# Kernel tuning notes

Hardware: AMD Instinct MI355X
Metric: run time of the kernel (lower is better)

Reference implementation:

```python
import jax, jax.numpy as jnp
import numpy as np

E = 1024  # embedding == hidden size
L = 2     # layer_num
S = 128   # sentence_length == seq_len
B = 64
LABEL = 5


def setup_inputs() -> dict:
    key = jax.random.key(0)
    ks = jax.random.split(key, 20)
    sc = 1.0 / np.sqrt(2 * E)
    def lin(k, i, o):
        kw, kb = jax.random.split(k)
        return (jax.random.uniform(kw, (i, o), jnp.float32, -sc, sc),
                jax.random.uniform(kb, (o,), jnp.float32, -sc, sc))
    # per-direction stacked gate weights [L, 2E, E]
    def gates(k):
        kk = jax.random.split(k, 3 * L)
        Ws, bs = [], []
        for g in range(3):
            W = jnp.stack([lin(kk[g * L + l], 2 * E, E)[0] for l in range(L)])
            b = jnp.stack([lin(jax.random.fold_in(kk[g * L + l], 7), 2 * E, E)[1] for l in range(L)])
            Ws.append(W); bs.append(b)
        return Ws, bs
    (fW, fb) = gates(ks[0])
    (bW, bb) = gates(ks[1])
    word_W, word_b = lin(ks[2], 2 * E, 1)
    pw = 1.0 / np.sqrt(S)
    pred_W = jax.random.uniform(ks[3], (S, LABEL), jnp.float32, -pw, pw)
    pred_b = jax.random.uniform(ks[4], (LABEL,), jnp.float32, -pw, pw)
    return {
        "inputs": jax.random.normal(ks[5], (B, S, E), jnp.float32),
        "cell_states": jnp.zeros((B, E), jnp.float32),
        "hidden_states": jnp.zeros((B, E), jnp.float32),
        "back_states": jnp.zeros((B, E), jnp.float32),
        "back_hidden": jnp.zeros((B, E), jnp.float32),
        "fWf": fW[0], "fbf": fb[0], "fWi": fW[1], "fbi": fb[1], "fWc": fW[2], "fbc": fb[2],
        "bWf": bW[0], "bbf": bb[0], "bWi": bW[1], "bbi": bb[1], "bWc": bW[2], "bbc": bb[2],
        "word_W": word_W, "word_b": word_b, "pred_W": pred_W, "pred_b": pred_b,
    }


def _run_dir(x_seq, h0, c0, Wf, bf, Wi, bi, Wc, bc):
    # x_seq: [S,B,E]; h0,c0: [B,E] broadcast to all layers
    hc0 = (jnp.broadcast_to(h0, (L,) + h0.shape), jnp.broadcast_to(c0, (L,) + c0.shape))
    def step(carry, x_t):
        h, c = carry
        inp = x_t
        hs, cs = [], []
        for l in range(L):
            z = jnp.concatenate([h[l], inp], axis=-1)       # [B,2E]
            f = jax.nn.sigmoid(z @ Wf[l] + bf[l])
            i = jax.nn.sigmoid(z @ Wi[l] + bi[l])
            g = jnp.tanh(z @ Wc[l] + bc[l])
            c_new = c[l] * f + i * g
            h_new = jnp.tanh(c_new) * f                     # note: forget gate reused as output gate (as in source)
            hs.append(h_new); cs.append(c_new); inp = h_new
        return (jnp.stack(hs), jnp.stack(cs)), inp
    _, out = jax.lax.scan(step, hc0, x_seq)
    return out  # [S,B,E]


def reference(inputs, cell_states, hidden_states, back_states, back_hidden,
              fWf, fbf, fWi, fbi, fWc, fbc,
              bWf, bbf, bWi, bbi, bWc, bbc,
              word_W, word_b, pred_W, pred_b):
    x = jnp.transpose(inputs, (1, 0, 2))                     # [S,B,E]
    fwd = _run_dir(x, hidden_states, cell_states, fWf, fbf, fWi, fbi, fWc, fbc)
    bwd = _run_dir(x[::-1], hidden_states, cell_states, bWf, bbf, bWi, bbi, bWc, bbc)[::-1]
    out = jnp.concatenate([fwd, bwd], axis=-1)               # [S,B,2E]
    out = jnp.transpose(out, (1, 0, 2))                      # [B,S,2E]
    w = (out @ word_W + word_b).reshape(out.shape[0], -1)    # [B,S]
    return w @ pred_W + pred_b                               # [B,LABEL]
```

## Files before the change

kernel.cpp:

```cpp
#include <hip/hip_runtime.h>
#include <cstddef>
#include <cstdint>

typedef _Float16 half8 __attribute__((ext_vector_type(8)));
typedef float f32x4 __attribute__((ext_vector_type(4)));

#define S_LEN 128
#define B_SZ  64
#define E_SZ  1024
#define NLBL  5
#define NPHASE 129

#define WOFF_WREC  0ull
#define WOFF_WINP  25165824ull
#define WOFF_X16   50331648ull
#define M0_H0    67108864ull
#define M0_H1    100925440ull
#define M0_WPART 134742016ull
#define M0_W     138936320ull
#define M0_FLAGS 138969088ull
#define NEED0    139001856ull
#define M1_H0    67108864ull
#define M1_H1    67633152ull
#define M1_WPART 68157440ull
#define M1_W     72351744ull
#define M1_FLAGS 72384512ull
#define NEED1    72417280ull

struct PP {
  const float* x;
  const float* W[2][3];
  const float* bias[2][3];
  const float* wordW;
  const float* cs0;
  _Float16* wrec;
  _Float16* winp;
  _Float16* x16;
  _Float16* h0;
  _Float16* h1;
  float* w;
  float* wpart;
  int* flags;
};

__device__ __forceinline__ uint32_t pack2f16(float a, float b) {
  return (uint32_t)__builtin_bit_cast(unsigned short, (_Float16)a) |
         ((uint32_t)__builtin_bit_cast(unsigned short, (_Float16)b) << 16);
}

#define MFMA16(A, B, C) __builtin_amdgcn_mfma_f32_16x16x32_f16(A, B, C, 0, 0, 0)

#define S_ISSUE_A4C(Q, P0, P1, P2, P3)                                     \
  asm volatile("global_load_dwordx4 %0, %4, off sc0 sc1\n\t"               \
               "global_load_dwordx4 %1, %5, off sc0 sc1\n\t"               \
               "global_load_dwordx4 %2, %6, off sc0 sc1\n\t"               \
               "global_load_dwordx4 %3, %7, off sc0 sc1"                   \
               : "=&v"((Q)[0]), "=&v"((Q)[1]), "=&v"((Q)[2]), "=&v"((Q)[3]) \
               : "v"(P0), "v"(P1), "v"(P2), "v"(P3))

#define S_ISSUE_A4P(Q, P0, P1, P2, P3)                                     \
  asm volatile("global_load_dwordx4 %0, %4, off\n\t"                       \
               "global_load_dwordx4 %1, %5, off\n\t"                       \
               "global_load_dwordx4 %2, %6, off\n\t"                       \
               "global_load_dwordx4 %3, %7, off"                           \
               : "=&v"((Q)[0]), "=&v"((Q)[1]), "=&v"((Q)[2]), "=&v"((Q)[3]) \
               : "v"(P0), "v"(P1), "v"(P2), "v"(P3))

#define S_WAITV(N)                                                         \
  asm volatile("s_waitcnt vmcnt(" #N ")" ::: "memory");                    \
  __builtin_amdgcn_sched_barrier(0)

__device__ __forceinline__ void comp_rec2s(const uint4* q, int kcA,
                                           const _Float16* wlds, int l64,
                                           f32x4 acc[3][2]) {
  #pragma unroll
  for (int s = 0; s < 2; ++s) {
    const int kc = kcA + s;
    const half8 a0 = __builtin_bit_cast(half8, q[s * 2 + 0]);
    const half8 a1 = __builtin_bit_cast(half8, q[s * 2 + 1]);
    #pragma unroll
    for (int g = 0; g < 3; ++g) {
      const half8 bf = *(const half8*)(wlds + ((size_t)(g * 32 + kc) * 64 + l64) * 8);
      acc[g][0] = MFMA16(a0, bf, acc[g][0]);
      acc[g][1] = MFMA16(a1, bf, acc[g][1]);
    }
  }
}

__device__ __forceinline__ void comp_inp2(const uint4* aq, const uint4* wq,
                                          f32x4 acc[3][2]) {
  #pragma unroll
  for (int s = 0; s < 2; ++s) {
    const half8 a0 = __builtin_bit_cast(half8, aq[s * 2 + 0]);
    const half8 a1 = __builtin_bit_cast(half8, aq[s * 2 + 1]);
    #pragma unroll
    for (int g = 0; g < 3; ++g) {
      const half8 bf = __builtin_bit_cast(half8, wq[s * 3 + g]);
      acc[g][0] = MFMA16(a0, bf, acc[g][0]);
      acc[g][1] = MFMA16(a1, bf, acc[g][1]);
    }
  }
}

__global__ __launch_bounds__(256)
void conv_w_kernel(PP p) {
  const int blk = blockIdx.x;
  const int part = blk & 1;
  const int j16 = (blk >> 1) & 63;
  const int rest = blk >> 7;
  const int g = rest % 3;
  const int dl = rest / 3;
  const int l = dl & 1, d = dl >> 1;
  const int tid = threadIdx.x;
  const int l2 = tid & 63, kc0 = tid >> 6;
  const float* W = p.W[d][g] + (size_t)l * 2048 * 1024 + (size_t)(part ? 1024 : 0) * 1024;
  _Float16* out = (part ? p.winp : p.wrec) + (size_t)(dl * 64 + j16) * 49152 + (size_t)g * 16384;
  const int j = j16 * 16 + (l2 & 15);
  const int kbase = (l2 >> 4) * 8;
  #pragma unroll
  for (int ki = 0; ki < 8; ++ki) {
    const int kc = kc0 * 8 + ki;
    const int k0 = kc * 32 + kbase;
    half8 h;
    #pragma unroll
    for (int e2 = 0; e2 < 8; ++e2) h[e2] = (_Float16)W[(size_t)(k0 + e2) * 1024 + j];
    *(half8*)(out + ((size_t)kc * 64 + l2) * 8) = h;
  }
}

__global__ __launch_bounds__(256)
void conv_x_kernel(const float* x, _Float16* x16) {
  const size_t i8 = ((size_t)blockIdx.x * 256 + threadIdx.x) * 8;
  float4 a = *(const float4*)(x + i8);
  float4 b = *(const float4*)(x + i8 + 4);
  half8 h;
  h[0] = (_Float16)a.x; h[1] = (_Float16)a.y; h[2] = (_Float16)a.z; h[3] = (_Float16)a.w;
  h[4] = (_Float16)b.x; h[5] = (_Float16)b.y; h[6] = (_Float16)b.z; h[7] = (_Float16)b.w;
  *(half8*)(x16 + i8) = h;
}

template<int MODE>
__global__ __launch_bounds__(256)
void init2_kernel(PP p, const float* hs) {
  const size_t HU = (MODE == 0) ? 65536 : 131072;
  const size_t i = (size_t)blockIdx.x * 256 + threadIdx.x;
  if (i < 2 * HU) {
    const size_t ai = (i < HU) ? i : i - HU;
    _Float16* dst = (i < HU) ? p.h0 : p.h1;
    const size_t grp = ai >> 15;
    const size_t be = ai & 32767;
    const size_t b = be >> 9, ec = be & 511;
    const uint32_t v = pack2f16(hs[b * 1024 + ec * 2], hs[b * 1024 + ec * 2 + 1]);
    const size_t u32off = (MODE == 0) ? (grp * 129 * 32768 + be) : (grp * 32768 + be);
    ((uint32_t*)dst)[u32off] = v;
  } else if (i < 2 * HU + 8192) {
    p.flags[i - 2 * HU] = 0;
  }
}

template<int MODE>
__global__ __launch_bounds__(512, 2)
void lstm_persist(PP p) {
  extern __shared__ char smem[];
  _Float16* wlds = (_Float16*)smem;
  float* pre  = (float*)(smem + 98304);
  float* wred = (float*)(smem + 150528);

  const int tid = threadIdx.x;
  const int l64 = tid & 63, lr = l64 & 15, lg = l64 >> 4;
  const int wv = tid >> 6, kq = wv & 3, mg = wv >> 2;
  const int blk = blockIdx.x;
  const int j16 = blk & 63, l = (blk >> 6) & 1, d = blk >> 7;
  const int idx = blk & 127;
  const int j0 = j16 * 16;

  if (tid == 0)
    (void)__hip_atomic_load(p.flags, __ATOMIC_ACQUIRE, __HIP_MEMORY_SCOPE_AGENT);
  __syncthreads();

  const size_t tileoff = (size_t)((d * 2 + l) * 64 + j16) * 49152;
  {
    const float4* src = (const float4*)(p.wrec + tileoff);
    float4* dst = (float4*)wlds;
    #pragma unroll
    for (int i = 0; i < 12; ++i) dst[tid + i * 512] = src[tid + i * 512];
  }
  const _Float16* wtile = p.winp + tileoff;
  _Float16* hrec_arr = l ? p.h1 : p.h0;

  uint4 wreg[24];
  #pragma unroll
  for (int i = 0; i < 24; ++i) {
    const int kcl = i / 3, g = i % 3;
    const int kc = kq * 8 + kcl;
    wreg[i] = *(const uint4*)(wtile + ((size_t)(g * 32 + kc) * 64 + l64) * 8);
  }

  const int pr = tid >> 3;
  const int pj = (tid & 7) * 2;
  const int pjg = j0 + pj;
  const float bsf0 = p.bias[d][0][l * E_SZ + pjg], bsf1 = p.bias[d][0][l * E_SZ + pjg + 1];
  const float bsi0 = p.bias[d][1][l * E_SZ + pjg], bsi1 = p.bias[d][1][l * E_SZ + pjg + 1];
  const float bsc0 = p.bias[d][2][l * E_SZ + pjg], bsc1 = p.bias[d][2][l * E_SZ + pjg + 1];
  const float ww0 = p.wordW[d * E_SZ + pjg], ww1 = p.wordW[d * E_SZ + pjg + 1];
  float creg0 = p.cs0[(size_t)pr * E_SZ + pjg];
  float creg1 = p.cs0[(size_t)pr * E_SZ + pjg + 1];
  __syncthreads();

  auto hoff = [&](int dd, int s) -> size_t {
    return (MODE == 0) ? ((size_t)dd * 129 + s) * 65536 : ((size_t)(dd * 2 + s)) * 65536;
  };

  for (int ph = 0; ph < NPHASE; ++ph) {
    const int t = l ? (ph - 1) : ph;
    if ((unsigned)t < (unsigned)S_LEN) {
      const int par = t & 1, prev = par ^ 1;
      const int td = d ? (S_LEN - 1 - t) : t;
      const int rs    = (MODE == 0) ? t : prev;
      const int wslot = (MODE == 0) ? (t + 1) : par;
      const int islot = (MODE == 0) ? (t + 1) : par;

      const _Float16* hAf = hrec_arr + hoff(d, rs);
      const _Float16* r0 = hAf + (size_t)(mg * 32 + lr) * 1024;
      const _Float16* r1 = hAf + (size_t)(mg * 32 + 16 + lr) * 1024;
      const _Float16* a0base;
      const _Float16* a1base;
      if (l == 0) {
        a0base = p.x16 + ((size_t)(mg * 32 + lr) * S_LEN + td) * 1024;
        a1base = p.x16 + ((size_t)(mg * 32 + 16 + lr) * S_LEN + td) * 1024;
      } else {
        const _Float16* hf = p.h0 + hoff(d, islot);
        a0base = hf + (size_t)(mg * 32 + lr) * 1024;
        a1base = hf + (size_t)(mg * 32 + 16 + lr) * 1024;
      }

      const f32x4 zero = {0.f, 0.f, 0.f, 0.f};
      f32x4 acc[3][2];
      #pragma unroll
      for (int g = 0; g < 3; ++g) { acc[g][0] = zero; acc[g][1] = zero; }

      auto issue_rec = [&](int c, uint4* Q) {
        const int kk = (kq * 8 + c * 2) * 32 + lg * 8;
        if (MODE == 0) {
          S_ISSUE_A4P(Q, r0 + kk, r1 + kk, r0 + kk + 32, r1 + kk + 32);
        } else {
          S_ISSUE_A4C(Q, r0 + kk, r1 + kk, r0 + kk + 32, r1 + kk + 32);
        }
      };
      auto issue_a = [&](int c, uint4* Q) {
        const int kk = (kq * 8 + c * 2) * 32 + lg * 8;
        if (MODE == 0 || l == 0) {
          S_ISSUE_A4P(Q, a0base + kk, a1base + kk, a0base + kk + 32, a1base + kk + 32);
        } else {
          S_ISSUE_A4C(Q, a0base + kk, a1base + kk, a0base + kk + 32, a1base + kk + 32);
        }
      };

      uint4 b0[4], b1[4], b2[4];
      issue_rec(0, b0); issue_rec(1, b1); issue_rec(2, b2);
      S_WAITV(8); comp_rec2s(b0, kq * 8 + 0, wlds, l64, acc); issue_rec(3, b0);
      S_WAITV(8); comp_rec2s(b1, kq * 8 + 2, wlds, l64, acc); issue_a(0, b1);
      S_WAITV(8); comp_rec2s(b2, kq * 8 + 4, wlds, l64, acc); issue_a(1, b2);
      S_WAITV(8); comp_rec2s(b0, kq * 8 + 6, wlds, l64, acc); issue_a(2, b0);
      S_WAITV(8); comp_inp2(b1, &wreg[0],  acc); issue_a(3, b1);
      S_WAITV(8); comp_inp2(b2, &wreg[6],  acc);
      S_WAITV(4); comp_inp2(b0, &wreg[12], acc);
      S_WAITV(0); comp_inp2(b1, &wreg[18], acc);

      #pragma unroll
      for (int g = 0; g < 3; ++g)
        #pragma unroll
        for (int mt = 0; mt < 2; ++mt)
          #pragma unroll
          for (int pp = 0; pp < 4; ++pp)
            pre[(((kq * 3 + g) * 64) + (mg * 2 + mt) * 16 + lg * 4 + pp) * 17 + lr] =
                acc[g][mt][pp];
      __syncthreads();

      float fp0 = bsf0, fp1 = bsf1, ip0 = bsi0, ip1 = bsi1, cp0 = bsc0, cp1 = bsc1;
      #pragma unroll
      for (int k = 0; k < 4; ++k) {
        fp0 += pre[((k * 3 + 0) * 64 + pr) * 17 + pj];
        fp1 += pre[((k * 3 + 0) * 64 + pr) * 17 + pj + 1];
        ip0 += pre[((k * 3 + 1) * 64 + pr) * 17 + pj];
        ip1 += pre[((k * 3 + 1) * 64 + pr) * 17 + pj + 1];
        cp0 += pre[((k * 3 + 2) * 64 + pr) * 17 + pj];
        cp1 += pre[((k * 3 + 2) * 64 + pr) * 17 + pj + 1];
      }
      const float fg0 = 1.f / (1.f + expf(-fp0)), fg1 = 1.f / (1.f + expf(-fp1));
      const float ig0 = 1.f / (1.f + expf(-ip0)), ig1 = 1.f / (1.f + expf(-ip1));
      const float gg0 = tanhf(cp0), gg1 = tanhf(cp1);
      creg0 = creg0 * fg0 + ig0 * gg0;
      creg1 = creg1 * fg1 + ig1 * gg1;
      const float h0v = tanhf(creg0) * fg0;
      const float h1v = tanhf(creg1) * fg1;

      uint32_t* hdst = (uint32_t*)(hrec_arr + hoff(d, wslot) + (size_t)pr * 1024 + pjg);
      const uint32_t pk = pack2f16(h0v, h1v);
      asm volatile("global_store_dword %0, %1, off sc0 sc1" ::"v"(hdst), "v"(pk) : "memory");
      if (l) {
        wred[pr * 16 + pj] = h0v * ww0;
        wred[pr * 16 + pj + 1] = h1v * ww1;
        __syncthreads();
        if (tid < 64) {
          float s = 0.f;
          #pragma unroll
          for (int q = 0; q < 16; ++q) s += wred[tid * 16 + q];
          p.wpart[((size_t)(d * 64 + j16) * S_LEN + td) * 64 + tid] = s;
        }
      }
    }

    __syncthreads();
    if (tid == 0) {
      __hip_atomic_store(p.flags + (size_t)(d * 128 + idx) * 32, ph + 1,
                         __ATOMIC_RELAXED, __HIP_MEMORY_SCOPE_AGENT);
      asm volatile("s_waitcnt vmcnt(0)" ::: "memory");
    }
    if (tid < 128) {
      const int* fl = p.flags + (size_t)(d * 128 + tid) * 32;
      int f, it = 0;
      do {
        f = __hip_atomic_load(fl, __ATOMIC_RELAXED, __HIP_MEMORY_SCOPE_AGENT);
        if (f >= ph + 1) break;
        __builtin_amdgcn_s_sleep(1);
      } while (++it < (1 << 22));
    }
    __syncthreads();
  }
}

__global__ __launch_bounds__(64)
void reduce_w_kernel(const float* wpart, const float* wordb, float* w) {
  const int t = blockIdx.x, b = threadIdx.x;
  float s = wordb[0];
  #pragma unroll 8
  for (int q = 0; q < 128; ++q)
    s += wpart[((size_t)q * S_LEN + t) * 64 + b];
  w[b * S_LEN + t] = s;
}

__global__ __launch_bounds__(320)
void final_kernel(const float* w, const float* predW, const float* predb, float* out) {
  const int tid = threadIdx.x;
  if (tid >= B_SZ * NLBL) return;
  const int b = tid / NLBL, lab = tid % NLBL;
  float s = predb[lab];
  #pragma unroll 8
  for (int t = 0; t < S_LEN; ++t) s += w[b * S_LEN + t] * predW[t * NLBL + lab];
  out[tid] = s;
}

extern "C" void kernel_launch(void* const* d_in, const int* in_sizes, int n_in,
                              void* d_out, int out_size, void* d_ws, size_t ws_size,
                              hipStream_t stream) {
  char* ws = (char*)d_ws;
  const bool hist = (ws_size >= NEED0);

  PP p;
  p.x = (const float*)d_in[0];
  p.W[0][0] = (const float*)d_in[5];  p.bias[0][0] = (const float*)d_in[6];
  p.W[0][1] = (const float*)d_in[7];  p.bias[0][1] = (const float*)d_in[8];
  p.W[0][2] = (const float*)d_in[9];  p.bias[0][2] = (const float*)d_in[10];
  p.W[1][0] = (const float*)d_in[11]; p.bias[1][0] = (const float*)d_in[12];
  p.W[1][1] = (const float*)d_in[13]; p.bias[1][1] = (const float*)d_in[14];
  p.W[1][2] = (const float*)d_in[15]; p.bias[1][2] = (const float*)d_in[16];
  p.wordW = (const float*)d_in[17];
  p.cs0   = (const float*)d_in[1];
  p.wrec  = (_Float16*)(ws + WOFF_WREC);
  p.winp  = (_Float16*)(ws + WOFF_WINP);
  p.x16   = (_Float16*)(ws + WOFF_X16);
  if (hist) {
    p.h0    = (_Float16*)(ws + M0_H0);
    p.h1    = (_Float16*)(ws + M0_H1);
    p.wpart = (float*)(ws + M0_WPART);
    p.w     = (float*)(ws + M0_W);
    p.flags = (int*)(ws + M0_FLAGS);
  } else {
    p.h0    = (_Float16*)(ws + M1_H0);
    p.h1    = (_Float16*)(ws + M1_H1);
    p.wpart = (float*)(ws + M1_WPART);
    p.w     = (float*)(ws + M1_W);
    p.flags = (int*)(ws + M1_FLAGS);
  }

  hipFuncSetAttribute(reinterpret_cast<const void*>(&lstm_persist<0>),
                      hipFuncAttributeMaxDynamicSharedMemorySize, 155648);
  hipFuncSetAttribute(reinterpret_cast<const void*>(&lstm_persist<1>),
                      hipFuncAttributeMaxDynamicSharedMemorySize, 155648);

  conv_w_kernel<<<1536, 256, 0, stream>>>(p);
  conv_x_kernel<<<4096, 256, 0, stream>>>(p.x, p.x16);
  if (hist) {
    init2_kernel<0><<<544, 256, 0, stream>>>(p, (const float*)d_in[2]);
    lstm_persist<0><<<256, 512, 155648, stream>>>(p);
  } else {
    init2_kernel<1><<<1056, 256, 0, stream>>>(p, (const float*)d_in[2]);
    lstm_persist<1><<<256, 512, 155648, stream>>>(p);
  }
  reduce_w_kernel<<<128, 64, 0, stream>>>(p.wpart, (const float*)d_in[18], p.w);
  final_kernel<<<1, 320, 0, stream>>>(p.w, (const float*)d_in[19],
                                      (const float*)d_in[20], (float*)d_out);
}
```

Measured before the change: 1.360 ms.

## Prefetch next-step x before barrier, publish flags early, narrow waits, fast activations

Layer-0 blocks now prefetch half of the next timestep's input x before the inter-block spin wait. The first two input-projection MFMA chunks then run from registers while the recurrent loads are still in flight. The flag store now happens right after the gate math, before the word-projection partial reduction, and layer-0 blocks in MODE 0 wait only on the 64 layer-0 flags. Sigmoid and tanh use __expf-based approximations. Together these aim to shorten the serialized per-step critical path of the persistent recurrent kernel, at some cost in activation accuracy and register pressure.

```diff
diff --git a/kernel.cpp b/kernel.cpp
--- a/kernel.cpp
+++ b/kernel.cpp
@@ -46,6 +46,13 @@
 __device__ __forceinline__ uint32_t pack2f16(float a, float b) {
   return (uint32_t)__builtin_bit_cast(unsigned short, (_Float16)a) |
          ((uint32_t)__builtin_bit_cast(unsigned short, (_Float16)b) << 16);
+}
+
+__device__ __forceinline__ float fast_sigmoid(float x) {
+  return 1.f / (1.f + __expf(-x));
+}
+__device__ __forceinline__ float fast_tanh(float x) {
+  return 1.f - 2.f / (__expf(2.f * x) + 1.f);
 }
 
 #define MFMA16(A, B, C) __builtin_amdgcn_mfma_f32_16x16x32_f16(A, B, C, 0, 0, 0)
@@ -211,9 +218,24 @@
     return (MODE == 0) ? ((size_t)dd * 129 + s) * 65536 : ((size_t)(dd * 2 + s)) * 65536;
   };
 
+  const _Float16* xr0 = p.x16 + (size_t)(mg * 32 + lr) * S_LEN * 1024;
+  const _Float16* xr1 = p.x16 + (size_t)(mg * 32 + 16 + lr) * S_LEN * 1024;
+
+  uint4 xq0[4], xq1[4];
+  if (l == 0) {
+    const int tdn = d ? (S_LEN - 1) : 0;
+    const _Float16* a0 = xr0 + (size_t)tdn * 1024;
+    const _Float16* a1 = xr1 + (size_t)tdn * 1024;
+    const int kk0 = (kq * 8 + 0) * 32 + lg * 8;
+    const int kk1 = (kq * 8 + 2) * 32 + lg * 8;
+    S_ISSUE_A4P(xq0, a0 + kk0, a1 + kk0, a0 + kk0 + 32, a1 + kk0 + 32);
+    S_ISSUE_A4P(xq1, a0 + kk1, a1 + kk1, a0 + kk1 + 32, a1 + kk1 + 32);
+  }
+
   for (int ph = 0; ph < NPHASE; ++ph) {
     const int t = l ? (ph - 1) : ph;
-    if ((unsigned)t < (unsigned)S_LEN) {
+    const bool active = (unsigned)t < (unsigned)S_LEN;
+    if (active) {
       const int par = t & 1, prev = par ^ 1;
       const int td = d ? (S_LEN - 1 - t) : t;
       const int rs    = (MODE == 0) ? t : prev;
@@ -223,16 +245,6 @@
       const _Float16* hAf = hrec_arr + hoff(d, rs);
       const _Float16* r0 = hAf + (size_t)(mg * 32 + lr) * 1024;
       const _Float16* r1 = hAf + (size_t)(mg * 32 + 16 + lr) * 1024;
-      const _Float16* a0base;
-      const _Float16* a1base;
-      if (l == 0) {
-        a0base = p.x16 + ((size_t)(mg * 32 + lr) * S_LEN + td) * 1024;
-        a1base = p.x16 + ((size_t)(mg * 32 + 16 + lr) * S_LEN + td) * 1024;
-      } else {
-        const _Float16* hf = p.h0 + hoff(d, islot);
-        a0base = hf + (size_t)(mg * 32 + lr) * 1024;
-        a1base = hf + (size_t)(mg * 32 + 16 + lr) * 1024;
-      }
 
       const f32x4 zero = {0.f, 0.f, 0.f, 0.f};
       f32x4 acc[3][2];
@@ -247,25 +259,46 @@
           S_ISSUE_A4C(Q, r0 + kk, r1 + kk, r0 + kk + 32, r1 + kk + 32);
         }
       };
-      auto issue_a = [&](int c, uint4* Q) {
-        const int kk = (kq * 8 + c * 2) * 32 + lg * 8;
-        if (MODE == 0 || l == 0) {
+
+      uint4 b0[4], b1[4], b2[4];
+      if (l == 0) {
+        const _Float16* a0base = xr0 + (size_t)td * 1024;
+        const _Float16* a1base = xr1 + (size_t)td * 1024;
+        auto issue_x = [&](int c, uint4* Q) {
+          const int kk = (kq * 8 + c * 2) * 32 + lg * 8;
           S_ISSUE_A4P(Q, a0base + kk, a1base + kk, a0base + kk + 32, a1base + kk + 32);
-        } else {
-          S_ISSUE_A4C(Q, a0base + kk, a1base + kk, a0base + kk + 32, a1base + kk + 32);
-        }
-      };
-
-      uint4 b0[4], b1[4], b2[4];
-      issue_rec(0, b0); issue_rec(1, b1); issue_rec(2, b2);
-      S_WAITV(8); comp_rec2s(b0, kq * 8 + 0, wlds, l64, acc); issue_rec(3, b0);
-      S_WAITV(8); comp_rec2s(b1, kq * 8 + 2, wlds, l64, acc); issue_a(0, b1);
-      S_WAITV(8); comp_rec2s(b2, kq * 8 + 4, wlds, l64, acc); issue_a(1, b2);
-      S_WAITV(8); comp_rec2s(b0, kq * 8 + 6, wlds, l64, acc); issue_a(2, b0);
-      S_WAITV(8); comp_inp2(b1, &wreg[0],  acc); issue_a(3, b1);
-      S_WAITV(8); comp_inp2(b2, &wreg[6],  acc);
-      S_WAITV(4); comp_inp2(b0, &wreg[12], acc);
-      S_WAITV(0); comp_inp2(b1, &wreg[18], acc);
+        };
+        issue_rec(0, b0); issue_rec(1, b1); issue_rec(2, b2);
+        comp_inp2(xq0, &wreg[0], acc);
+        comp_inp2(xq1, &wreg[6], acc);
+        S_WAITV(8);  comp_rec2s(b0, kq * 8 + 0, wlds, l64, acc); issue_rec(3, b0);
+        S_WAITV(8);  comp_rec2s(b1, kq * 8 + 2, wlds, l64, acc); issue_x(2, b1);
+        S_WAITV(8);  comp_rec2s(b2, kq * 8 + 4, wlds, l64, acc); issue_x(3, b2);
+        S_WAITV(8);  comp_rec2s(b0, kq * 8 + 6, wlds, l64, acc);
+        S_WAITV(4);  comp_inp2(b1, &wreg[12], acc);
+        S_WAITV(0);  comp_inp2(b2, &wreg[18], acc);
+      } else {
+        const _Float16* hf = p.h0 + hoff(d, islot);
+        const _Float16* a0base = hf + (size_t)(mg * 32 + lr) * 1024;
+        const _Float16* a1base = hf + (size_t)(mg * 32 + 16 + lr) * 1024;
+        auto issue_a = [&](int c, uint4* Q) {
+          const int kk = (kq * 8 + c * 2) * 32 + lg * 8;
+          if (MODE == 0) {
+            S_ISSUE_A4P(Q, a0base + kk, a1base + kk, a0base + kk + 32, a1base + kk + 32);
+          } else {
+            S_ISSUE_A4C(Q, a0base + kk, a1base + kk, a0base + kk + 32, a1base + kk + 32);
+          }
+        };
+        issue_rec(0, b0); issue_rec(1, b1); issue_rec(2, b2);
+        S_WAITV(8); comp_rec2s(b0, kq * 8 + 0, wlds, l64, acc); issue_rec(3, b0);
+        S_WAITV(8); comp_rec2s(b1, kq * 8 + 2, wlds, l64, acc); issue_a(0, b1);
+        S_WAITV(8); comp_rec2s(b2, kq * 8 + 4, wlds, l64, acc); issue_a(1, b2);
+        S_WAITV(8); comp_rec2s(b0, kq * 8 + 6, wlds, l64, acc); issue_a(2, b0);
+        S_WAITV(8); comp_inp2(b1, &wreg[0],  acc); issue_a(3, b1);
+        S_WAITV(8); comp_inp2(b2, &wreg[6],  acc);
+        S_WAITV(4); comp_inp2(b0, &wreg[12], acc);
+        S_WAITV(0); comp_inp2(b1, &wreg[18], acc);
+      }
 
       #pragma unroll
       for (int g = 0; g < 3; ++g)
@@ -287,13 +320,13 @@
         cp0 += pre[((k * 3 + 2) * 64 + pr) * 17 + pj];
         cp1 += pre[((k * 3 + 2) * 64 + pr) * 17 + pj + 1];
       }
-      const float fg0 = 1.f / (1.f + expf(-fp0)), fg1 = 1.f / (1.f + expf(-fp1));
-      const float ig0 = 1.f / (1.f + expf(-ip0)), ig1 = 1.f / (1.f + expf(-ip1));
-      const float gg0 = tanhf(cp0), gg1 = tanhf(cp1);
+      const float fg0 = fast_sigmoid(fp0), fg1 = fast_sigmoid(fp1);
+      const float ig0 = fast_sigmoid(ip0), ig1 = fast_sigmoid(ip1);
+      const float gg0 = fast_tanh(cp0), gg1 = fast_tanh(cp1);
       creg0 = creg0 * fg0 + ig0 * gg0;
       creg1 = creg1 * fg1 + ig1 * gg1;
-      const float h0v = tanhf(creg0) * fg0;
-      const float h1v = tanhf(creg1) * fg1;
+      const float h0v = fast_tanh(creg0) * fg0;
+      const float h1v = fast_tanh(creg1) * fg1;
 
       uint32_t* hdst = (uint32_t*)(hrec_arr + hoff(d, wslot) + (size_t)pr * 1024 + pjg);
       const uint32_t pk = pack2f16(h0v, h1v);
@@ -301,30 +334,51 @@
       if (l) {
         wred[pr * 16 + pj] = h0v * ww0;
         wred[pr * 16 + pj + 1] = h1v * ww1;
-        __syncthreads();
-        if (tid < 64) {
-          float s = 0.f;
-          #pragma unroll
-          for (int q = 0; q < 16; ++q) s += wred[tid * 16 + q];
-          p.wpart[((size_t)(d * 64 + j16) * S_LEN + td) * 64 + tid] = s;
-        }
+      }
+      __syncthreads();
+      if (tid == 0) {
+        __hip_atomic_store(p.flags + (size_t)(d * 128 + idx) * 32, ph + 1,
+                           __ATOMIC_RELAXED, __HIP_MEMORY_SCOPE_AGENT);
+        asm volatile("s_waitcnt vmcnt(0)" ::: "memory");
+      }
+      if (l && tid < 64) {
+        const int tdw = d ? (S_LEN - 1 - t) : t;
+        float s = 0.f;
+        #pragma unroll
+        for (int q = 0; q < 16; ++q) s += wred[tid * 16 + q];
+        p.wpart[((size_t)(d * 64 + j16) * S_LEN + tdw) * 64 + tid] = s;
+      }
+    } else {
+      __syncthreads();
+      if (tid == 0) {
+        __hip_atomic_store(p.flags + (size_t)(d * 128 + idx) * 32, ph + 1,
+                           __ATOMIC_RELAXED, __HIP_MEMORY_SCOPE_AGENT);
+        asm volatile("s_waitcnt vmcnt(0)" ::: "memory");
       }
     }
 
-    __syncthreads();
-    if (tid == 0) {
-      __hip_atomic_store(p.flags + (size_t)(d * 128 + idx) * 32, ph + 1,
-                         __ATOMIC_RELAXED, __HIP_MEMORY_SCOPE_AGENT);
-      asm volatile("s_waitcnt vmcnt(0)" ::: "memory");
+    if (l == 0 && ph + 1 < S_LEN) {
+      const int tn = ph + 1;
+      const int tdn = d ? (S_LEN - 1 - tn) : tn;
+      const _Float16* a0 = xr0 + (size_t)tdn * 1024;
+      const _Float16* a1 = xr1 + (size_t)tdn * 1024;
+      const int kk0 = (kq * 8 + 0) * 32 + lg * 8;
+      const int kk1 = (kq * 8 + 2) * 32 + lg * 8;
+      S_ISSUE_A4P(xq0, a0 + kk0, a1 + kk0, a0 + kk0 + 32, a1 + kk0 + 32);
+      S_ISSUE_A4P(xq1, a0 + kk1, a1 + kk1, a0 + kk1 + 32, a1 + kk1 + 32);
     }
-    if (tid < 128) {
-      const int* fl = p.flags + (size_t)(d * 128 + tid) * 32;
-      int f, it = 0;
-      do {
-        f = __hip_atomic_load(fl, __ATOMIC_RELAXED, __HIP_MEMORY_SCOPE_AGENT);
-        if (f >= ph + 1) break;
-        __builtin_amdgcn_s_sleep(1);
-      } while (++it < (1 << 22));
+
+    {
+      const int nflags = (MODE == 0 && l == 0) ? 64 : 128;
+      if (tid < nflags) {
+        const int* fl = p.flags + (size_t)(d * 128 + tid) * 32;
+        int f, it = 0;
+        do {
+          f = __hip_atomic_load(fl, __ATOMIC_RELAXED, __HIP_MEMORY_SCOPE_AGENT);
+          if (f >= ph + 1) break;
+          __builtin_amdgcn_s_sleep(1);
+        } while (++it < (1 << 22));
+      }
     }
     __syncthreads();
   }
```

After: 1.448 ms. 6.4% more time.
